# Optimization experiments

Hardware: AMD Instinct MI355X
Metric: run time of the kernel (lower is better)

## Reference

```python
import jax, jax.numpy as jnp
import numpy as np

D_MODEL = 1024
NUM_HEADS = 16
D_HEAD = D_MODEL // NUM_HEADS  # 64, used only as softmax scale
DFF = 4096
EPS = 1e-6


def _layernorm(x, gamma, beta):
    mu = jnp.mean(x, axis=-1, keepdims=True)
    var = jnp.mean(jnp.square(x - mu), axis=-1, keepdims=True)
    return (x - mu) * jax.lax.rsqrt(var + EPS) * gamma + beta


def _mha(q_in, kv, score, Wq, bq, Wk, bk, Wv, bv, Wo, bo):
    # q_in: [B,Sq,d]; kv: [Sv,d] (broadcast over batch, mirroring unsqueeze(0))
    Q = q_in @ Wq.T + bq                      # [B,Sq,d]
    K = kv @ Wk.T + bk                        # [Sv,d]
    V = kv @ Wv.T + bv                        # [Sv,d]
    scores = (jnp.einsum('bqd,kd->bqk', Q, K) + score) / jnp.sqrt(
        jnp.asarray(D_HEAD, dtype=jnp.float32))
    w = jax.nn.softmax(scores, axis=-1)       # [B,Sq,Sv]
    out = jnp.einsum('bqk,kd->bqd', w, V)     # [B,Sq,d]
    return out @ Wo.T + bo


def setup_inputs() -> dict:
    key = jax.random.key(0)
    ks = jax.random.split(key, 20)
    B, Sq, Sv = 4, 2048, 196
    s = 0.02
    inp = {
        'text_tensor': jax.random.normal(ks[0], (B, Sq, D_MODEL), jnp.float32),
        'visual_tensor': jax.random.normal(ks[1], (Sv, D_MODEL), jnp.float32),
        'score_matrix': jax.random.normal(ks[2], (B, Sq, Sv), jnp.float32),
        'text_tensor2': jax.random.normal(ks[3], (B, Sq, D_MODEL), jnp.float32),
        'visual_tensor2': jax.random.normal(ks[4], (Sv, D_MODEL), jnp.float32),
        'score_matrix2': jax.random.normal(ks[5], (B, Sq, Sv), jnp.float32),
        'Wq': jax.random.normal(ks[6], (D_MODEL, D_MODEL), jnp.float32) * s,
        'bq': jnp.zeros((D_MODEL,), jnp.float32),
        'Wk': jax.random.normal(ks[7], (D_MODEL, D_MODEL), jnp.float32) * s,
        'bk': jnp.zeros((D_MODEL,), jnp.float32),
        'Wv': jax.random.normal(ks[8], (D_MODEL, D_MODEL), jnp.float32) * s,
        'bv': jnp.zeros((D_MODEL,), jnp.float32),
        'Wo': jax.random.normal(ks[9], (D_MODEL, D_MODEL), jnp.float32) * s,
        'bo': jnp.zeros((D_MODEL,), jnp.float32),
        'W1': jax.random.normal(ks[10], (DFF, D_MODEL), jnp.float32) * s,
        'b1': jnp.zeros((DFF,), jnp.float32),
        'W2': jax.random.normal(ks[11], (D_MODEL, DFF), jnp.float32) * s,
        'b2': jnp.zeros((D_MODEL,), jnp.float32),
        'g1': jnp.ones((D_MODEL,), jnp.float32),
        'be1': jnp.zeros((D_MODEL,), jnp.float32),
        'g2': jnp.ones((D_MODEL,), jnp.float32),
        'be2': jnp.zeros((D_MODEL,), jnp.float32),
    }
    return inp


def reference(text_tensor, visual_tensor, score_matrix,
              text_tensor2, visual_tensor2, score_matrix2,
              Wq, bq, Wk, bk, Wv, bv, Wo, bo,
              W1, b1, W2, b2, g1, be1, g2, be2):
    # Branch 1 (dropout is identity in eval mode)
    a1 = _mha(text_tensor, visual_tensor, score_matrix,
              Wq, bq, Wk, bk, Wv, bv, Wo, bo)
    out1 = _layernorm(text_tensor + a1, g1, be1)
    # Branch 2 (shared attention weights, same layernorm1)
    a2 = _mha(text_tensor2, visual_tensor2, score_matrix2,
              Wq, bq, Wk, bk, Wv, bv, Wo, bo)
    out2 = _layernorm(text_tensor2 + a2, g1, be1)
    # Concat along features then MaxPool1d(kernel=2, stride=2) over last dim
    concat = jnp.concatenate([out1, out2], axis=2)       # [B,Sq,2d]
    B, Sq, _ = concat.shape
    pooled = jnp.max(concat.reshape(B, Sq, D_MODEL, 2), axis=-1)  # [B,Sq,d]
    # FFN + residual + layernorm2
    ffn = jax.nn.relu(pooled @ W1.T + b1) @ W2.T + b2
    return _layernorm(pooled + ffn, g2, be2)
```

## Files before the change

### kernel.cpp

```cpp
#include <hip/hip_runtime.h>
#include <hip/hip_bf16.h>
#include <cstdint>
#include <type_traits>

typedef unsigned short u16;
typedef __bf16 bf16x8 __attribute__((ext_vector_type(8)));
typedef float f32x4 __attribute__((ext_vector_type(4)));

#define LN_EPS 1e-6f

enum { BIAS_NONE = 0, BIAS_COL = 1, BIAS_ROW = 2 };

__device__ __forceinline__ float b2f(u16 h) {
  union { unsigned u; float f; } v;
  v.u = ((unsigned)h) << 16;
  return v.f;
}
__device__ __forceinline__ u16 f2b(float x) {
  return __bfloat16_as_ushort(__float2bfloat16(x));
}

__device__ __forceinline__ void gld_lds16(const void* g, void* l) {
  __builtin_amdgcn_global_load_lds(
      (const __attribute__((address_space(1))) void*)g,
      (__attribute__((address_space(3))) void*)l, 16, 0, 0);
}

__device__ __forceinline__ void st8(float4 a, float4 b, u16* dst) {
  u16 t[8] = {f2b(a.x), f2b(a.y), f2b(a.z), f2b(a.w),
              f2b(b.x), f2b(b.y), f2b(b.z), f2b(b.w)};
  *reinterpret_cast<uint4*>(dst) = *reinterpret_cast<const uint4*>(t);
}

__device__ __forceinline__ void stage8_cvt(const float* src, size_t off,
                                           u16* dst) {
  const float* p = src + off;
  st8(*reinterpret_cast<const float4*>(p),
      *reinterpret_cast<const float4*>(p + 4), dst);
}

template <typename OutT, int BIAS, bool RELU, bool A_RAW, bool B_RAW, int TM,
          int TN>
__global__ __launch_bounds__(256, 2) void gemm_db(
    const void* __restrict__ A, const void* __restrict__ A2,
    const void* __restrict__ B, const void* __restrict__ B2,
    const float* __restrict__ bias, const float* __restrict__ bias2,
    OutT* __restrict__ C, int M, int N, int K, int MA, int NB, int ldc,
    int Msplit, int bias_and) {
  constexpr int SA = TM / 64;
  constexpr int SB = TN / 64;
  constexpr int AI = (TM == 128 && TN == 128) ? 4 : 2;
  constexpr int BJ = (TM == 64 && TN == 64) ? 2 : 4;
  __shared__ __align__(16) u16 As[2][TM * 32];
  __shared__ __align__(16) u16 Bs[2][TN * 32];
  const int tid = threadIdx.x;
  const int lane = tid & 63;
  const int wv = tid >> 6;
  int wr, wc;
  if constexpr (TM == 128 && TN == 128) {
    wr = (wv >> 1) * 64; wc = (wv & 1) * 64;
  } else if constexpr (TM == 128 && TN == 64) {
    wr = wv * 32; wc = 0;
  } else {
    wr = (wv >> 1) * 32; wc = (wv & 1) * 32;
  }
  const int mrow = lane & 15;
  const int quad = lane >> 4;

  int bxi = blockIdx.x, byi = blockIdx.y;
  {
    const int gx = (int)gridDim.x;
    const int nwg = gx * (int)gridDim.y;
    if ((nwg & 7) == 0) {
      int wg = byi * gx + bxi;
      wg = (wg & 7) * (nwg >> 3) + (wg >> 3);
      bxi = wg % gx;
      byi = wg / gx;
    }
  }
  const int bm = byi * TM;
  const int bn = bxi * TN;

  f32x4 acc[AI][BJ];
#pragma unroll
  for (int i = 0; i < AI; i++)
#pragma unroll
    for (int j = 0; j < BJ; j++) acc[i][j] = f32x4{0.f, 0.f, 0.f, 0.f};

  const int e0 = tid * 8;
  const int r0 = e0 >> 5;
  const int sw0 = ((((e0 >> 3) & 3) ^ ((r0 >> 1) & 3)) << 3);

  const void* Asrc[SA];
  size_t aoff[SA];
#pragma unroll
  for (int s = 0; s < SA; s++) {
    int ra = bm + r0 + s * 64;
    if (ra >= MA) ra = MA - 1;
    Asrc[s] = (ra < Msplit) ? A : A2;
    const int rr = (ra < Msplit) ? ra : ra - Msplit;
    aoff[s] = (size_t)rr * K + sw0;
  }
  const void* Bb = (bm < Msplit) ? B : B2;
  size_t boff[SB];
#pragma unroll
  for (int s = 0; s < SB; s++) {
    int rb = bn + r0 + s * 64;
    if (rb >= NB) rb = NB - 1;
    boff[s] = (size_t)rb * K + sw0;
  }

#pragma unroll
  for (int s = 0; s < SA; s++) {
    if constexpr (A_RAW) {
      const float* p = (const float*)Asrc[s] + aoff[s];
      st8(*reinterpret_cast<const float4*>(p),
          *reinterpret_cast<const float4*>(p + 4), &As[0][e0 + s * 2048]);
    } else {
      gld_lds16((const u16*)Asrc[s] + aoff[s], &As[0][e0 + s * 2048]);
    }
  }
#pragma unroll
  for (int s = 0; s < SB; s++) {
    if constexpr (B_RAW) {
      const float* p = (const float*)Bb + boff[s];
      st8(*reinterpret_cast<const float4*>(p),
          *reinterpret_cast<const float4*>(p + 4), &Bs[0][e0 + s * 2048]);
    } else {
      gld_lds16((const u16*)Bb + boff[s], &Bs[0][e0 + s * 2048]);
    }
  }
  __syncthreads();

  const int so = ((quad ^ ((mrow >> 1) & 3)) << 3);

  int cur = 0;
  for (int k0 = 0; k0 < K; k0 += 32) {
    const int nk = k0 + 32;
    const bool pf = nk < K;
    float4 fA[SA][2], fB[SB][2];
    if (pf) {
#pragma unroll
      for (int s = 0; s < SA; s++) {
        if constexpr (A_RAW) {
          const float* p = (const float*)Asrc[s] + aoff[s] + nk;
          fA[s][0] = *reinterpret_cast<const float4*>(p);
          fA[s][1] = *reinterpret_cast<const float4*>(p + 4);
        } else {
          gld_lds16((const u16*)Asrc[s] + aoff[s] + nk,
                    &As[cur ^ 1][e0 + s * 2048]);
        }
      }
#pragma unroll
      for (int s = 0; s < SB; s++) {
        if constexpr (B_RAW) {
          const float* p = (const float*)Bb + boff[s] + nk;
          fB[s][0] = *reinterpret_cast<const float4*>(p);
          fB[s][1] = *reinterpret_cast<const float4*>(p + 4);
        } else {
          gld_lds16((const u16*)Bb + boff[s] + nk, &Bs[cur ^ 1][e0 + s * 2048]);
        }
      }
    }
    bf16x8 af[AI], bfm[BJ];
#pragma unroll
    for (int i = 0; i < AI; i++)
      af[i] = *reinterpret_cast<const bf16x8*>(
          &As[cur][(wr + i * 16 + mrow) * 32 + so]);
#pragma unroll
    for (int j = 0; j < BJ; j++)
      bfm[j] = *reinterpret_cast<const bf16x8*>(
          &Bs[cur][(wc + j * 16 + mrow) * 32 + so]);
#pragma unroll
    for (int i = 0; i < AI; i++)
#pragma unroll
      for (int j = 0; j < BJ; j++)
        acc[i][j] = __builtin_amdgcn_mfma_f32_16x16x32_bf16(af[i], bfm[j],
                                                            acc[i][j], 0, 0, 0);
    if (pf) {
      if constexpr (A_RAW) {
#pragma unroll
        for (int s = 0; s < SA; s++)
          st8(fA[s][0], fA[s][1], &As[cur ^ 1][e0 + s * 2048]);
      }
      if constexpr (B_RAW) {
#pragma unroll
        for (int s = 0; s < SB; s++)
          st8(fB[s][0], fB[s][1], &Bs[cur ^ 1][e0 + s * 2048]);
      }
    }
    __syncthreads();
    cur ^= 1;
  }

  const float* bp = (bm < Msplit) ? bias : bias2;
#pragma unroll
  for (int i = 0; i < AI; i++) {
#pragma unroll
    for (int j = 0; j < BJ; j++) {
#pragma unroll
      for (int r = 0; r < 4; r++) {
        const int gr = bm + wr + i * 16 + quad * 4 + r;
        const int gc = bn + wc + j * 16 + mrow;
        if (gr < M && gc < N) {
          float v = acc[i][j][r];
          if (BIAS == BIAS_COL) v += bp[gc];
          if (BIAS == BIAS_ROW) v += bp[gr & bias_and];
          if (RELU) v = fmaxf(v, 0.f);
          if constexpr (std::is_same<OutT, float>::value)
            C[(size_t)gr * ldc + gc] = v;
          else
            C[(size_t)gr * ldc + gc] = f2b(v);
        }
      }
    }
  }
}

__global__ __launch_bounds__(256) void cvt_k(const float* __restrict__ src,
                                             u16* __restrict__ dst, int n8) {
  const int i = blockIdx.x * 256 + threadIdx.x;
  if (i >= n8) return;
  stage8_cvt(src, (size_t)i * 8, dst + (size_t)i * 8);
}

__global__ __launch_bounds__(256) void wqt_k(const float* __restrict__ src,
                                             u16* __restrict__ dst) {
  __shared__ float t[64][65];
  const int bx = blockIdx.x;
  const int by = blockIdx.y;
  const int tx = threadIdx.x & 63;
  const int ty = threadIdx.x >> 6;
#pragma unroll
  for (int i = 0; i < 16; i++)
    t[ty * 16 + i][tx] =
        src[(size_t)(by * 64 + ty * 16 + i) * 1024 + bx * 64 + tx];
  __syncthreads();
#pragma unroll
  for (int i = 0; i < 16; i++)
    dst[(size_t)(bx * 64 + ty * 16 + i) * 1024 + by * 64 + tx] =
        f2b(t[tx][ty * 16 + i]);
}

__global__ __launch_bounds__(256) void kb_k(const u16* __restrict__ Kc,
                                            const float* __restrict__ bq,
                                            float* __restrict__ kb) {
  const int wvi = blockIdx.x * 4 + (threadIdx.x >> 6);
  const int lane = threadIdx.x & 63;
  const int b = wvi / 224, s = wvi % 224;
  float sum = 0.f;
  if (s < 196) {
    const u16* row = Kc + (size_t)(b * 196 + s) * 1024;
    for (int j = lane; j < 1024; j += 64) sum += b2f(row[j]) * bq[j];
  }
#pragma unroll
  for (int off = 32; off > 0; off >>= 1) sum += __shfl_xor(sum, off);
  if (lane == 0) kb[wvi] = sum;
}

__global__ __launch_bounds__(256) void softmax_k(
    u16* __restrict__ Sp, const float* __restrict__ sc1,
    const float* __restrict__ sc2) {
  const int row = blockIdx.x * 4 + (threadIdx.x >> 6);
  const int lane = threadIdx.x & 63;
  const float* score = (row < 8192) ? sc1 + (size_t)row * 196
                                    : sc2 + (size_t)(row - 8192) * 196;
  float x[4];
  float mx = -1e30f;
#pragma unroll
  for (int t = 0; t < 4; t++) {
    const int s = lane + 64 * t;
    float v = -1e30f;
    if (s < 196) v = (b2f(Sp[(size_t)row * 224 + s]) + score[s]) * 0.125f;
    x[t] = v;
    mx = fmaxf(mx, v);
  }
#pragma unroll
  for (int off = 32; off > 0; off >>= 1) mx = fmaxf(mx, __shfl_xor(mx, off));
  float sum = 0.f;
#pragma unroll
  for (int t = 0; t < 4; t++) {
    const int s = lane + 64 * t;
    const float e = (s < 196) ? expf(x[t] - mx) : 0.f;
    x[t] = e;
    sum += e;
  }
#pragma unroll
  for (int off = 32; off > 0; off >>= 1) sum += __shfl_xor(sum, off);
  const float inv = 1.f / sum;
#pragma unroll
  for (int t = 0; t < 4; t++) {
    const int s = lane + 64 * t;
    if (s < 224) Sp[(size_t)row * 224 + s] = f2b((s < 196) ? x[t] * inv : 0.f);
  }
}

__global__ __launch_bounds__(256) void ln_pool_k(
    const float* __restrict__ X, const u16* __restrict__ Y,
    const float* __restrict__ g, const float* __restrict__ be,
    u16* __restrict__ pooled, int colbase) {
  const int row = blockIdx.x;
  const int tid = threadIdx.x;
  const int lane = tid & 63;
  const int wv = tid >> 6;
  __shared__ float red[4];
  float v[4];
  float s = 0.f;
  const size_t base = (size_t)row * 1024 + tid * 4;
#pragma unroll
  for (int j = 0; j < 4; j++) {
    const float a = X[base + j] + b2f(Y[base + j]);
    v[j] = a;
    s += a;
  }
#pragma unroll
  for (int off = 32; off > 0; off >>= 1) s += __shfl_xor(s, off);
  if (lane == 0) red[wv] = s;
  __syncthreads();
  const float mu = (red[0] + red[1] + red[2] + red[3]) * (1.f / 1024.f);
  __syncthreads();
  float var = 0.f;
#pragma unroll
  for (int j = 0; j < 4; j++) {
    const float d = v[j] - mu;
    var += d * d;
  }
#pragma unroll
  for (int off = 32; off > 0; off >>= 1) var += __shfl_xor(var, off);
  if (lane == 0) red[wv] = var;
  __syncthreads();
  var = (red[0] + red[1] + red[2] + red[3]) * (1.f / 1024.f);
  const float rs = rsqrtf(var + LN_EPS);
  float n[4];
#pragma unroll
  for (int j = 0; j < 4; j++)
    n[j] = (v[j] - mu) * rs * g[tid * 4 + j] + be[tid * 4 + j];
  const size_t pb = (size_t)row * 1024 + colbase + tid * 2;
  pooled[pb] = f2b(fmaxf(n[0], n[1]));
  pooled[pb + 1] = f2b(fmaxf(n[2], n[3]));
}

__global__ __launch_bounds__(256) void ln_out_k(
    const u16* __restrict__ X, const u16* __restrict__ Y,
    const float* __restrict__ g, const float* __restrict__ be,
    float* __restrict__ out) {
  const int row = blockIdx.x;
  const int tid = threadIdx.x;
  const int lane = tid & 63;
  const int wv = tid >> 6;
  __shared__ float red[4];
  float v[4];
  float s = 0.f;
  const size_t base = (size_t)row * 1024 + tid * 4;
#pragma unroll
  for (int j = 0; j < 4; j++) {
    const float a = b2f(X[base + j]) + b2f(Y[base + j]);
    v[j] = a;
    s += a;
  }
#pragma unroll
  for (int off = 32; off > 0; off >>= 1) s += __shfl_xor(s, off);
  if (lane == 0) red[wv] = s;
  __syncthreads();
  const float mu = (red[0] + red[1] + red[2] + red[3]) * (1.f / 1024.f);
  __syncthreads();
  float var = 0.f;
#pragma unroll
  for (int j = 0; j < 4; j++) {
    const float d = v[j] - mu;
    var += d * d;
  }
#pragma unroll
  for (int off = 32; off > 0; off >>= 1) var += __shfl_xor(var, off);
  if (lane == 0) red[wv] = var;
  __syncthreads();
  var = (red[0] + red[1] + red[2] + red[3]) * (1.f / 1024.f);
  const float rs = rsqrtf(var + LN_EPS);
#pragma unroll
  for (int j = 0; j < 4; j++)
    out[base + j] = (v[j] - mu) * rs * g[tid * 4 + j] + be[tid * 4 + j];
}

extern "C" void kernel_launch(void* const* d_in, const int* in_sizes, int n_in,
                              void* d_out, int out_size, void* d_ws,
                              size_t ws_size, hipStream_t stream) {
  const size_t MB = 1ull << 20;
  if (ws_size < 61 * MB) return;

  const float* text1 = (const float*)d_in[0];
  const float* vis1 = (const float*)d_in[1];
  const float* sc1 = (const float*)d_in[2];
  const float* text2 = (const float*)d_in[3];
  const float* vis2 = (const float*)d_in[4];
  const float* sc2 = (const float*)d_in[5];
  const float* Wq = (const float*)d_in[6];
  const float* bq = (const float*)d_in[7];
  const float* Wk = (const float*)d_in[8];
  const float* bk = (const float*)d_in[9];
  const float* Wv = (const float*)d_in[10];
  const float* bv = (const float*)d_in[11];
  const float* Wo = (const float*)d_in[12];
  const float* bo = (const float*)d_in[13];
  const float* W1 = (const float*)d_in[14];
  const float* b1 = (const float*)d_in[15];
  const float* W2 = (const float*)d_in[16];
  const float* b2 = (const float*)d_in[17];
  const float* g1 = (const float*)d_in[18];
  const float* be1 = (const float*)d_in[19];
  const float* g2 = (const float*)d_in[20];
  const float* be2 = (const float*)d_in[21];

  const int D = 1024, Sv = 196, SvP = 224, DFF = 4096;
  const int M2 = 16384;
  char* w = (char*)d_ws;
  u16* pooled = (u16*)(w + 0 * MB);
  u16* Wkb = (u16*)(w + 16 * MB);
  u16* Wvb = (u16*)(w + 18 * MB);
  u16* Wob = (u16*)(w + 20 * MB);
  u16* WqT = (u16*)(w + 22 * MB);
  u16* Kcat = (u16*)(w + 24 * MB);
  u16* Vcat = (u16*)(w + 25 * MB);
  u16* K2cat = (u16*)(w + 26 * MB);
  u16* VWoT = (u16*)(w + 27 * MB);
  float* kb = (float*)(w + 28 * MB);
  u16* Spcat = (u16*)(w + 29 * MB);
  u16* Ocat = (u16*)d_out;
  u16* H = (u16*)(w + 16 * MB);
  u16* F = (u16*)(w + 48 * MB);
  u16* W1b = (u16*)((char*)d_out + 16 * MB);
  u16* W2b = (u16*)((char*)d_out + 24 * MB);

  auto grid = [](int m, int n, int tm, int tn) {
    return dim3((unsigned)((n + tn - 1) / tn), (unsigned)((m + tm - 1) / tm));
  };
  auto cgrid = [](int n) { return dim3((unsigned)((n / 8 + 255) / 256)); };

  cvt_k<<<cgrid(D * D), 256, 0, stream>>>(Wk, Wkb, D * D / 8);
  cvt_k<<<cgrid(D * D), 256, 0, stream>>>(Wv, Wvb, D * D / 8);
  cvt_k<<<cgrid(D * D), 256, 0, stream>>>(Wo, Wob, D * D / 8);
  wqt_k<<<dim3(16, 16), 256, 0, stream>>>(Wq, WqT);

  gemm_db<u16, BIAS_COL, false, true, false, 64, 64>
      <<<grid(2 * Sv, D, 64, 64), 256, 0, stream>>>(
          vis1, vis2, Wkb, Wkb, bk, bk, Kcat, 2 * Sv, D, D, 2 * Sv, D, D, Sv,
          0);
  gemm_db<u16, BIAS_COL, false, true, false, 64, 64>
      <<<grid(2 * Sv, D, 64, 64), 256, 0, stream>>>(
          vis1, vis2, Wvb, Wvb, bv, bv, Vcat, 2 * Sv, D, D, 2 * Sv, D, D, Sv,
          0);
  gemm_db<u16, BIAS_NONE, false, false, false, 64, 64>
      <<<grid(2 * Sv, D, 64, 64), 256, 0, stream>>>(
          Kcat, Kcat, WqT, WqT, nullptr, nullptr, K2cat, 2 * Sv, D, D, 2 * Sv,
          D, D, 2 * Sv, 0);
  kb_k<<<dim3(112), 256, 0, stream>>>(Kcat, bq, kb);
  gemm_db<u16, BIAS_COL, false, true, false, 64, 64>
      <<<grid(M2, Sv, 64, 64), 256, 0, stream>>>(
          text1, text2, K2cat, K2cat + (size_t)Sv * D, kb, kb + SvP, Spcat, M2,
          Sv, D, M2, Sv, SvP, 8192, 0);
  softmax_k<<<dim3(M2 / 4), 256, 0, stream>>>(Spcat, sc1, sc2);
  gemm_db<u16, BIAS_ROW, false, false, false, 64, 64>
      <<<grid(2 * D, SvP, 64, 64), 256, 0, stream>>>(
          Wob, Wob, Vcat, Vcat + (size_t)Sv * D, bo, bo, VWoT, 2 * D, SvP, D,
          2 * D, Sv, SvP, D, D - 1);
  gemm_db<u16, BIAS_NONE, false, false, false, 128, 64>
      <<<grid(M2, D, 128, 64), 256, 0, stream>>>(
          Spcat, Spcat + (size_t)8192 * SvP, VWoT, VWoT + (size_t)D * SvP,
          nullptr, nullptr, Ocat, M2, D, SvP, M2, D, D, 8192, 0);
  ln_pool_k<<<dim3(8192), 256, 0, stream>>>(text1, Ocat, g1, be1, pooled, 0);
  ln_pool_k<<<dim3(8192), 256, 0, stream>>>(text2, Ocat + (size_t)8192 * D, g1,
                                            be1, pooled, 512);

  cvt_k<<<cgrid(DFF * D), 256, 0, stream>>>(W1, W1b, DFF * D / 8);
  cvt_k<<<cgrid(DFF * D), 256, 0, stream>>>(W2, W2b, DFF * D / 8);

  for (int c = 0; c < 2; ++c) {
    const int r0 = c * 4096, rows = 4096;
    gemm_db<u16, BIAS_COL, true, false, false, 128, 64>
        <<<grid(rows, DFF, 128, 64), 256, 0, stream>>>(
            pooled + (size_t)r0 * D, pooled + (size_t)r0 * D, W1b, W1b, b1, b1,
            H, rows, DFF, D, rows, DFF, DFF, rows, 0);
    gemm_db<u16, BIAS_COL, false, false, false, 64, 64>
        <<<grid(rows, D, 64, 64), 256, 0, stream>>>(H, H, W2b, W2b, b2, b2, F,
                                                    rows, D, DFF, rows, D, D,
                                                    rows, 0);
    ln_out_k<<<dim3(rows), 256, 0, stream>>>(
        pooled + (size_t)r0 * D, F, g2, be2, (float*)d_out + (size_t)r0 * D);
  }
}
```

Before: 624.6 us.

## Generalize GEMM tiling, fuse K/V projections, merge conversion and layernorm launches

The GEMM template gains a configurable K-step (BK) and thread count (NT), plus explicit lda/ldb. The FFN1 GEMM now runs with 128x128 tiles on 512 threads, and the FFN2 GEMM uses BK=64. The K and V projections are fused into one GEMM with a split column bias and an interleaved KVcat layout. The weight conversions are merged into multi-segment cvt3 launches, and the two layernorm-pool launches are merged into one. The aim is fewer launches and more reuse per tile, at the cost of more LDS and register pressure per block.

```diff
diff --git a/kernel.cpp b/kernel.cpp
--- a/kernel.cpp
+++ b/kernel.cpp
@@ -9,7 +9,7 @@
 
 #define LN_EPS 1e-6f
 
-enum { BIAS_NONE = 0, BIAS_COL = 1, BIAS_ROW = 2 };
+enum { BIAS_NONE = 0, BIAS_COL = 1, BIAS_ROW = 2, BIAS_COL2 = 3 };
 
 __device__ __forceinline__ float b2f(u16 h) {
   union { unsigned u; float f; } v;
@@ -40,24 +40,26 @@
 }
 
 template <typename OutT, int BIAS, bool RELU, bool A_RAW, bool B_RAW, int TM,
-          int TN>
-__global__ __launch_bounds__(256, 2) void gemm_db(
+          int TN, int BK, int NT>
+__global__ __launch_bounds__(NT, (NT == 512) ? 4 : 2) void gemm_db(
     const void* __restrict__ A, const void* __restrict__ A2,
     const void* __restrict__ B, const void* __restrict__ B2,
     const float* __restrict__ bias, const float* __restrict__ bias2,
-    OutT* __restrict__ C, int M, int N, int K, int MA, int NB, int ldc,
-    int Msplit, int bias_and) {
-  constexpr int SA = TM / 64;
-  constexpr int SB = TN / 64;
-  constexpr int AI = (TM == 128 && TN == 128) ? 4 : 2;
+    OutT* __restrict__ C, int M, int N, int K, int lda, int ldb, int MA,
+    int NB, int ldc, int Msplit, int rowmask, int colsplit) {
+  constexpr int SA = (TM * BK) / (NT * 8);
+  constexpr int SB = (TN * BK) / (NT * 8);
+  constexpr int AI = (NT == 512) ? 2 : ((TM == 128 && TN == 128) ? 4 : 2);
   constexpr int BJ = (TM == 64 && TN == 64) ? 2 : 4;
-  __shared__ __align__(16) u16 As[2][TM * 32];
-  __shared__ __align__(16) u16 Bs[2][TN * 32];
+  __shared__ __align__(16) u16 As[2][TM * BK];
+  __shared__ __align__(16) u16 Bs[2][TN * BK];
   const int tid = threadIdx.x;
   const int lane = tid & 63;
   const int wv = tid >> 6;
   int wr, wc;
-  if constexpr (TM == 128 && TN == 128) {
+  if constexpr (NT == 512) {
+    wr = (wv & 3) * 32; wc = (wv >> 2) * 64;
+  } else if constexpr (TM == 128 && TN == 128) {
     wr = (wv >> 1) * 64; wc = (wv & 1) * 64;
   } else if constexpr (TM == 128 && TN == 64) {
     wr = wv * 32; wc = 0;
@@ -88,26 +90,30 @@
     for (int j = 0; j < BJ; j++) acc[i][j] = f32x4{0.f, 0.f, 0.f, 0.f};
 
   const int e0 = tid * 8;
-  const int r0 = e0 >> 5;
-  const int sw0 = ((((e0 >> 3) & 3) ^ ((r0 >> 1) & 3)) << 3);
+  const int r0t = e0 >> 5;
+  const int swc8 = ((((e0 >> 3) & 3) ^ ((r0t >> 1) & 3)) << 3);
 
   const void* Asrc[SA];
   size_t aoff[SA];
 #pragma unroll
   for (int s = 0; s < SA; s++) {
-    int ra = bm + r0 + s * 64;
+    const int h = (s * NT * 8) / (TM * 32);
+    const int rb = ((s * NT * 8) % (TM * 32)) >> 5;
+    int ra = bm + rb + r0t;
     if (ra >= MA) ra = MA - 1;
     Asrc[s] = (ra < Msplit) ? A : A2;
     const int rr = (ra < Msplit) ? ra : ra - Msplit;
-    aoff[s] = (size_t)rr * K + sw0;
+    aoff[s] = (size_t)rr * lda + h * 32 + swc8;
   }
   const void* Bb = (bm < Msplit) ? B : B2;
   size_t boff[SB];
 #pragma unroll
   for (int s = 0; s < SB; s++) {
-    int rb = bn + r0 + s * 64;
-    if (rb >= NB) rb = NB - 1;
-    boff[s] = (size_t)rb * K + sw0;
+    const int h = (s * NT * 8) / (TN * 32);
+    const int rb = ((s * NT * 8) % (TN * 32)) >> 5;
+    int rbn = bn + rb + r0t;
+    if (rbn >= NB) rbn = NB - 1;
+    boff[s] = (size_t)rbn * ldb + h * 32 + swc8;
   }
 
 #pragma unroll
@@ -115,9 +121,9 @@
     if constexpr (A_RAW) {
       const float* p = (const float*)Asrc[s] + aoff[s];
       st8(*reinterpret_cast<const float4*>(p),
-          *reinterpret_cast<const float4*>(p + 4), &As[0][e0 + s * 2048]);
+          *reinterpret_cast<const float4*>(p + 4), &As[0][s * NT * 8 + e0]);
     } else {
-      gld_lds16((const u16*)Asrc[s] + aoff[s], &As[0][e0 + s * 2048]);
+      gld_lds16((const u16*)Asrc[s] + aoff[s], &As[0][s * NT * 8 + e0]);
     }
   }
 #pragma unroll
@@ -125,9 +131,9 @@
     if constexpr (B_RAW) {
       const float* p = (const float*)Bb + boff[s];
       st8(*reinterpret_cast<const float4*>(p),
-          *reinterpret_cast<const float4*>(p + 4), &Bs[0][e0 + s * 2048]);
+          *reinterpret_cast<const float4*>(p + 4), &Bs[0][s * NT * 8 + e0]);
     } else {
-      gld_lds16((const u16*)Bb + boff[s], &Bs[0][e0 + s * 2048]);
+      gld_lds16((const u16*)Bb + boff[s], &Bs[0][s * NT * 8 + e0]);
     }
   }
   __syncthreads();
@@ -135,8 +141,8 @@
   const int so = ((quad ^ ((mrow >> 1) & 3)) << 3);
 
   int cur = 0;
-  for (int k0 = 0; k0 < K; k0 += 32) {
-    const int nk = k0 + 32;
+  for (int k0 = 0; k0 < K; k0 += BK) {
+    const int nk = k0 + BK;
     const bool pf = nk < K;
     float4 fA[SA][2], fB[SB][2];
     if (pf) {
@@ -148,7 +154,7 @@
           fA[s][1] = *reinterpret_cast<const float4*>(p + 4);
         } else {
           gld_lds16((const u16*)Asrc[s] + aoff[s] + nk,
-                    &As[cur ^ 1][e0 + s * 2048]);
+                    &As[cur ^ 1][s * NT * 8 + e0]);
         }
       }
 #pragma unroll
@@ -158,35 +164,39 @@
           fB[s][0] = *reinterpret_cast<const float4*>(p);
           fB[s][1] = *reinterpret_cast<const float4*>(p + 4);
         } else {
-          gld_lds16((const u16*)Bb + boff[s] + nk, &Bs[cur ^ 1][e0 + s * 2048]);
+          gld_lds16((const u16*)Bb + boff[s] + nk,
+                    &Bs[cur ^ 1][s * NT * 8 + e0]);
         }
       }
     }
-    bf16x8 af[AI], bfm[BJ];
-#pragma unroll
-    for (int i = 0; i < AI; i++)
-      af[i] = *reinterpret_cast<const bf16x8*>(
-          &As[cur][(wr + i * 16 + mrow) * 32 + so]);
-#pragma unroll
-    for (int j = 0; j < BJ; j++)
-      bfm[j] = *reinterpret_cast<const bf16x8*>(
-          &Bs[cur][(wc + j * 16 + mrow) * 32 + so]);
-#pragma unroll
-    for (int i = 0; i < AI; i++)
+#pragma unroll
+    for (int h = 0; h < BK / 32; h++) {
+      bf16x8 af[AI], bfm[BJ];
+#pragma unroll
+      for (int i = 0; i < AI; i++)
+        af[i] = *reinterpret_cast<const bf16x8*>(
+            &As[cur][h * TM * 32 + (wr + i * 16 + mrow) * 32 + so]);
 #pragma unroll
       for (int j = 0; j < BJ; j++)
-        acc[i][j] = __builtin_amdgcn_mfma_f32_16x16x32_bf16(af[i], bfm[j],
-                                                            acc[i][j], 0, 0, 0);
+        bfm[j] = *reinterpret_cast<const bf16x8*>(
+            &Bs[cur][h * TN * 32 + (wc + j * 16 + mrow) * 32 + so]);
+#pragma unroll
+      for (int i = 0; i < AI; i++)
+#pragma unroll
+        for (int j = 0; j < BJ; j++)
+          acc[i][j] = __builtin_amdgcn_mfma_f32_16x16x32_bf16(
+              af[i], bfm[j], acc[i][j], 0, 0, 0);
+    }
     if (pf) {
       if constexpr (A_RAW) {
 #pragma unroll
         for (int s = 0; s < SA; s++)
-          st8(fA[s][0], fA[s][1], &As[cur ^ 1][e0 + s * 2048]);
+          st8(fA[s][0], fA[s][1], &As[cur ^ 1][s * NT * 8 + e0]);
       }
       if constexpr (B_RAW) {
 #pragma unroll
         for (int s = 0; s < SB; s++)
-          st8(fB[s][0], fB[s][1], &Bs[cur ^ 1][e0 + s * 2048]);
+          st8(fB[s][0], fB[s][1], &Bs[cur ^ 1][s * NT * 8 + e0]);
       }
     }
     __syncthreads();
@@ -205,7 +215,9 @@
         if (gr < M && gc < N) {
           float v = acc[i][j][r];
           if (BIAS == BIAS_COL) v += bp[gc];
-          if (BIAS == BIAS_ROW) v += bp[gr & bias_and];
+          if (BIAS == BIAS_COL2)
+            v += (gc < colsplit) ? bias[gc] : bias2[gc - colsplit];
+          if (BIAS == BIAS_ROW) v += bp[gr & rowmask];
           if (RELU) v = fmaxf(v, 0.f);
           if constexpr (std::is_same<OutT, float>::value)
             C[(size_t)gr * ldc + gc] = v;
@@ -217,11 +229,16 @@
   }
 }
 
-__global__ __launch_bounds__(256) void cvt_k(const float* __restrict__ src,
-                                             u16* __restrict__ dst, int n8) {
-  const int i = blockIdx.x * 256 + threadIdx.x;
-  if (i >= n8) return;
-  stage8_cvt(src, (size_t)i * 8, dst + (size_t)i * 8);
+__global__ __launch_bounds__(256) void cvt3_k(
+    const float* __restrict__ s0, u16* __restrict__ d0,
+    const float* __restrict__ s1, u16* __restrict__ d1,
+    const float* __restrict__ s2, u16* __restrict__ d2, int blocksPer) {
+  const int seg = blockIdx.x / blocksPer;
+  const int b = blockIdx.x % blocksPer;
+  const float* s = (seg == 0) ? s0 : ((seg == 1) ? s1 : s2);
+  u16* d = (seg == 0) ? d0 : ((seg == 1) ? d1 : d2);
+  const size_t i = ((size_t)b * 256 + threadIdx.x) * 8;
+  stage8_cvt(s, i, d + i);
 }
 
 __global__ __launch_bounds__(256) void wqt_k(const float* __restrict__ src,
@@ -244,13 +261,13 @@
 
 __global__ __launch_bounds__(256) void kb_k(const u16* __restrict__ Kc,
                                             const float* __restrict__ bq,
-                                            float* __restrict__ kb) {
+                                            float* __restrict__ kb, int ld) {
   const int wvi = blockIdx.x * 4 + (threadIdx.x >> 6);
   const int lane = threadIdx.x & 63;
   const int b = wvi / 224, s = wvi % 224;
   float sum = 0.f;
   if (s < 196) {
-    const u16* row = Kc + (size_t)(b * 196 + s) * 1024;
+    const u16* row = Kc + (size_t)(b * 196 + s) * ld;
     for (int j = lane; j < 1024; j += 64) sum += b2f(row[j]) * bq[j];
   }
 #pragma unroll
@@ -296,20 +313,23 @@
 }
 
 __global__ __launch_bounds__(256) void ln_pool_k(
-    const float* __restrict__ X, const u16* __restrict__ Y,
-    const float* __restrict__ g, const float* __restrict__ be,
-    u16* __restrict__ pooled, int colbase) {
-  const int row = blockIdx.x;
+    const float* __restrict__ X1, const float* __restrict__ X2,
+    const u16* __restrict__ Y, const float* __restrict__ g,
+    const float* __restrict__ be, u16* __restrict__ pooled) {
+  const int row16 = blockIdx.x;
+  const int br = row16 >> 13;
+  const int row = row16 & 8191;
   const int tid = threadIdx.x;
   const int lane = tid & 63;
   const int wv = tid >> 6;
+  const float* X = (br ? X2 : X1) + (size_t)row * 1024;
+  const u16* Yp = Y + (size_t)row16 * 1024;
   __shared__ float red[4];
   float v[4];
   float s = 0.f;
-  const size_t base = (size_t)row * 1024 + tid * 4;
 #pragma unroll
   for (int j = 0; j < 4; j++) {
-    const float a = X[base + j] + b2f(Y[base + j]);
+    const float a = X[tid * 4 + j] + b2f(Yp[tid * 4 + j]);
     v[j] = a;
     s += a;
   }
@@ -335,7 +355,7 @@
 #pragma unroll
   for (int j = 0; j < 4; j++)
     n[j] = (v[j] - mu) * rs * g[tid * 4 + j] + be[tid * 4 + j];
-  const size_t pb = (size_t)row * 1024 + colbase + tid * 2;
+  const size_t pb = (size_t)row * 1024 + br * 512 + tid * 2;
   pooled[pb] = f2b(fmaxf(n[0], n[1]));
   pooled[pb + 1] = f2b(fmaxf(n[2], n[3]));
 }
@@ -418,8 +438,7 @@
   u16* Wvb = (u16*)(w + 18 * MB);
   u16* Wob = (u16*)(w + 20 * MB);
   u16* WqT = (u16*)(w + 22 * MB);
-  u16* Kcat = (u16*)(w + 24 * MB);
-  u16* Vcat = (u16*)(w + 25 * MB);
+  u16* KVcat = (u16*)(w + 24 * MB);
   u16* K2cat = (u16*)(w + 26 * MB);
   u16* VWoT = (u16*)(w + 27 * MB);
   float* kb = (float*)(w + 28 * MB);
@@ -433,56 +452,46 @@
   auto grid = [](int m, int n, int tm, int tn) {
     return dim3((unsigned)((n + tn - 1) / tn), (unsigned)((m + tm - 1) / tm));
   };
-  auto cgrid = [](int n) { return dim3((unsigned)((n / 8 + 255) / 256)); };
-
-  cvt_k<<<cgrid(D * D), 256, 0, stream>>>(Wk, Wkb, D * D / 8);
-  cvt_k<<<cgrid(D * D), 256, 0, stream>>>(Wv, Wvb, D * D / 8);
-  cvt_k<<<cgrid(D * D), 256, 0, stream>>>(Wo, Wob, D * D / 8);
+
+  cvt3_k<<<dim3(3 * 512), 256, 0, stream>>>(Wk, Wkb, Wv, Wvb, Wo, Wob, 512);
   wqt_k<<<dim3(16, 16), 256, 0, stream>>>(Wq, WqT);
 
-  gemm_db<u16, BIAS_COL, false, true, false, 64, 64>
+  gemm_db<u16, BIAS_COL2, false, true, false, 64, 64, 32, 256>
+      <<<grid(2 * Sv, 2 * D, 64, 64), 256, 0, stream>>>(
+          vis1, vis2, Wkb, Wkb, bk, bv, KVcat, 2 * Sv, 2 * D, D, D, D, 2 * Sv,
+          2 * D, 2 * D, Sv, 0, D);
+  gemm_db<u16, BIAS_NONE, false, false, false, 64, 64, 32, 256>
       <<<grid(2 * Sv, D, 64, 64), 256, 0, stream>>>(
-          vis1, vis2, Wkb, Wkb, bk, bk, Kcat, 2 * Sv, D, D, 2 * Sv, D, D, Sv,
-          0);
-  gemm_db<u16, BIAS_COL, false, true, false, 64, 64>
-      <<<grid(2 * Sv, D, 64, 64), 256, 0, stream>>>(
-          vis1, vis2, Wvb, Wvb, bv, bv, Vcat, 2 * Sv, D, D, 2 * Sv, D, D, Sv,
-          0);
-  gemm_db<u16, BIAS_NONE, false, false, false, 64, 64>
-      <<<grid(2 * Sv, D, 64, 64), 256, 0, stream>>>(
-          Kcat, Kcat, WqT, WqT, nullptr, nullptr, K2cat, 2 * Sv, D, D, 2 * Sv,
-          D, D, 2 * Sv, 0);
-  kb_k<<<dim3(112), 256, 0, stream>>>(Kcat, bq, kb);
-  gemm_db<u16, BIAS_COL, false, true, false, 64, 64>
+          KVcat, KVcat, WqT, WqT, nullptr, nullptr, K2cat, 2 * Sv, D, D, 2 * D,
+          D, 2 * Sv, D, D, 2 * Sv, 0, 0);
+  kb_k<<<dim3(112), 256, 0, stream>>>(KVcat, bq, kb, 2 * D);
+  gemm_db<u16, BIAS_COL, false, true, false, 64, 64, 32, 256>
       <<<grid(M2, Sv, 64, 64), 256, 0, stream>>>(
           text1, text2, K2cat, K2cat + (size_t)Sv * D, kb, kb + SvP, Spcat, M2,
-          Sv, D, M2, Sv, SvP, 8192, 0);
+          Sv, D, D, D, M2, Sv, SvP, 8192, 0, 0);
   softmax_k<<<dim3(M2 / 4), 256, 0, stream>>>(Spcat, sc1, sc2);
-  gemm_db<u16, BIAS_ROW, false, false, false, 64, 64>
+  gemm_db<u16, BIAS_ROW, false, false, false, 64, 64, 32, 256>
       <<<grid(2 * D, SvP, 64, 64), 256, 0, stream>>>(
-          Wob, Wob, Vcat, Vcat + (size_t)Sv * D, bo, bo, VWoT, 2 * D, SvP, D,
-          2 * D, Sv, SvP, D, D - 1);
-  gemm_db<u16, BIAS_NONE, false, false, false, 128, 64>
+          Wob, Wob, KVcat + D, KVcat + (size_t)Sv * 2 * D + D, bo, bo, VWoT,
+          2 * D, SvP, D, D, 2 * D, 2 * D, Sv, SvP, D, D - 1, 0);
+  gemm_db<u16, BIAS_NONE, false, false, false, 128, 64, 32, 256>
       <<<grid(M2, D, 128, 64), 256, 0, stream>>>(
           Spcat, Spcat + (size_t)8192 * SvP, VWoT, VWoT + (size_t)D * SvP,
-          nullptr, nullptr, Ocat, M2, D, SvP, M2, D, D, 8192, 0);
-  ln_pool_k<<<dim3(8192), 256, 0, stream>>>(text1, Ocat, g1, be1, pooled, 0);
-  ln_pool_k<<<dim3(8192), 256, 0, stream>>>(text2, Ocat + (size_t)8192 * D, g1,
-                                            be1, pooled, 512);
-
-  cvt_k<<<cgrid(DFF * D), 256, 0, stream>>>(W1, W1b, DFF * D / 8);
-  cvt_k<<<cgrid(DFF * D), 256, 0, stream>>>(W2, W2b, DFF * D / 8);
+          nullptr, nullptr, Ocat, M2, D, SvP, SvP, SvP, M2, D, D, 8192, 0, 0);
+  ln_pool_k<<<dim3(M2), 256, 0, stream>>>(text1, text2, Ocat, g1, be1, pooled);
+
+  cvt3_k<<<dim3(2 * 2048), 256, 0, stream>>>(W1, W1b, W2, W2b, W2, W2b, 2048);
 
   for (int c = 0; c < 2; ++c) {
     const int r0 = c * 4096, rows = 4096;
-    gemm_db<u16, BIAS_COL, true, false, false, 128, 64>
-        <<<grid(rows, DFF, 128, 64), 256, 0, stream>>>(
+    gemm_db<u16, BIAS_COL, true, false, false, 128, 128, 32, 512>
+        <<<grid(rows, DFF, 128, 128), 512, 0, stream>>>(
             pooled + (size_t)r0 * D, pooled + (size_t)r0 * D, W1b, W1b, b1, b1,
-            H, rows, DFF, D, rows, DFF, DFF, rows, 0);
-    gemm_db<u16, BIAS_COL, false, false, false, 64, 64>
-        <<<grid(rows, D, 64, 64), 256, 0, stream>>>(H, H, W2b, W2b, b2, b2, F,
-                                                    rows, D, DFF, rows, D, D,
-                                                    rows, 0);
+            H, rows, DFF, D, D, D, rows, DFF, DFF, rows, 0, 0);
+    gemm_db<u16, BIAS_COL, false, false, false, 64, 64, 64, 256>
+        <<<grid(rows, D, 64, 64), 256, 0, stream>>>(
+            H, H, W2b, W2b, b2, b2, F, rows, D, DFF, DFF, DFF, rows, D, D,
+            rows, 0, 0);
     ln_out_k<<<dim3(rows), 256, 0, stream>>>(
         pooled + (size_t)r0 * D, F, g2, be2, (float*)d_out + (size_t)r0 * D);
   }
```

After: 544.6 us. 12.8% less time.
